# Kernel optimization log

Hardware: AMD Instinct MI355X
Metric: run time of the kernel (lower is better)

Reference implementation:

```python
import jax, jax.numpy as jnp
import numpy as np

N, C, H, W, D = 4, 320, 16, 16, 16
POS_RATIO = 0.5


def setup_inputs() -> dict:
    key = jax.random.key(0)
    k1, k2, k3, k4 = jax.random.split(key, 4)
    q = jax.random.normal(k1, (N, C, H, W, D), jnp.float32)
    k = jax.random.normal(k2, (N, C, H, W, D), jnp.float32)

    def make_coord(kr):
        # crop boxes: upper-left corner in [0, 0.4), extent in [0.4, 0.6)
        start = jax.random.uniform(kr, (N, 3), jnp.float32) * 0.4
        size = 0.4 + jax.random.uniform(jax.random.fold_in(kr, 1), (N, 3), jnp.float32) * 0.2
        return jnp.concatenate([start, start + size], axis=1)  # (N, 6)

    coord_q = make_coord(k3)
    coord_k = make_coord(k4)
    return {"q": q, "k": k, "coord_q": coord_q, "coord_k": coord_k}


def _centers(coord, h, w, d):
    """coord: (N,6) -> centers (N, h*w*d, 3) of each voxel in global coords, and bin diag (N,)."""
    dims = jnp.array([h, w, d], jnp.float32)
    bin_sz = (coord[:, 3:6] - coord[:, 0:3]) / dims  # (N,3) = (bin_h, bin_w, bin_d)
    ax = jnp.arange(h, dtype=jnp.float32) + 0.5
    ay = jnp.arange(w, dtype=jnp.float32) + 0.5
    az = jnp.arange(d, dtype=jnp.float32) + 0.5
    grid = jnp.stack(jnp.meshgrid(ax, ay, az, indexing="ij"), axis=-1)  # (h,w,d,3)
    grid = grid.reshape(1, h * w * d, 3)
    centers = grid * bin_sz[:, None, :] + coord[:, None, 0:3]  # (N, L, 3)
    diag = jnp.sqrt(jnp.sum(bin_sz ** 2, axis=-1))  # (N,)
    return centers, diag


def reference(q, k, coord_q, coord_k):
    n, c, h, w, d = q.shape
    L = h * w * d
    qf = q.reshape(n, c, L)
    kf = k.reshape(n, c, L)

    cq, diag_q = _centers(coord_q, h, w, d)  # (N,L,3), (N,)
    ck, diag_k = _centers(coord_k, h, w, d)
    max_diag = jnp.maximum(diag_q, diag_k)[:, None, None]  # (N,1,1)

    def masked_loss(q_flat, centers_q):
        # pairwise center distance (N, L, L) -- sum of three squared diffs, no (N,L,L,3) stack
        d2 = ((centers_q[:, :, None, 0] - ck[:, None, :, 0]) ** 2
              + (centers_q[:, :, None, 1] - ck[:, None, :, 1]) ** 2
              + (centers_q[:, :, None, 2] - ck[:, None, :, 2]) ** 2)
        dist = jnp.sqrt(d2) / max_diag
        mask = jax.lax.stop_gradient((dist < POS_RATIO).astype(jnp.float32))
        logit = jnp.einsum("ncl,ncm->nlm", q_flat, kf)  # bmm(q^T, k)
        return jnp.sum(logit * mask, axis=(-2, -1)) / (jnp.sum(mask, axis=(-2, -1)) + 1e-6)

    loss = masked_loss(qf, cq)
    # anatomy branch: flip(q) and flipped q-centers along batch dim 0 (as in source flip(x, dim=0))
    loss_rev = masked_loss(jnp.flip(qf, axis=0), jnp.flip(cq, axis=0))
    return -2.0 * jnp.mean(loss) - 2.0 * jnp.mean(loss_rev)
```

## Files before the change

kernel.cpp:

```cpp
#include <hip/hip_runtime.h>

#define LVOX   4096
#define NCH    320
#define NCOMBO 8
#define RCAP   49152
#define PKSTR  17
#define PKROW  (256 * PKSTR)
#define NBLK   (2 * NCH)
#define SPART_OFF 128
#define RUNS_OFF  (SPART_OFF + NCOMBO * NBLK * 4)

struct Geo {
    float qs0, qs1, qs2, qo0, qo1, qo2;
    float ks0, ks1, ks2, ko0, ko1, ko2;
    float ik0, ik1, ik2;
    float T;
};

__device__ __forceinline__ Geo make_geo(const float* __restrict__ cq,
                                        const float* __restrict__ ck,
                                        int n, int qb) {
    Geo g;
    const float* qc = cq + qb * 6;
    const float* qn = cq + n * 6;
    const float* kc = ck + n * 6;
    g.qs0 = (qc[3] - qc[0]) * (1.f / 16.f); g.qo0 = qc[0];
    g.qs1 = (qc[4] - qc[1]) * (1.f / 16.f); g.qo1 = qc[1];
    g.qs2 = (qc[5] - qc[2]) * (1.f / 16.f); g.qo2 = qc[2];
    g.ks0 = (kc[3] - kc[0]) * (1.f / 16.f); g.ko0 = kc[0];
    g.ks1 = (kc[4] - kc[1]) * (1.f / 16.f); g.ko1 = kc[1];
    g.ks2 = (kc[5] - kc[2]) * (1.f / 16.f); g.ko2 = kc[2];
    g.ik0 = 1.f / g.ks0; g.ik1 = 1.f / g.ks1; g.ik2 = 1.f / g.ks2;
    float b0 = (qn[3] - qn[0]) * (1.f / 16.f);
    float b1 = (qn[4] - qn[1]) * (1.f / 16.f);
    float b2 = (qn[5] - qn[2]) * (1.f / 16.f);
    float dq = sqrtf(b0 * b0 + b1 * b1 + b2 * b2);
    float dk = sqrtf(g.ks0 * g.ks0 + g.ks1 * g.ks1 + g.ks2 * g.ks2);
    g.T = 0.5f * fmaxf(dq, dk);
    return g;
}

__device__ __forceinline__ void axrange(float c, float ko, float ik, float T,
                                        int& m0, int& m1) {
    float lo = (c - T - ko) * ik - 0.5f;
    float hi = (c + T - ko) * ik - 0.5f;
    m0 = max((int)ceilf(lo) - 1, 0);
    m1 = min((int)floorf(hi) + 1, 15);
}

__global__ void enum_runs(const float* __restrict__ coord_q,
                          const float* __restrict__ coord_k,
                          unsigned* __restrict__ pcnt,
                          unsigned* __restrict__ rcnt,
                          unsigned* __restrict__ runs, int cap) {
    int gid = blockIdx.x * 256 + threadIdx.x;
    int j = gid >> 12;
    int l = gid & 4095;
    int n = j & 3;
    int qb = (j & 4) ? (3 - n) : n;
    Geo g = make_geo(coord_q, coord_k, n, qb);

    int ix = l >> 8, iy = (l >> 4) & 15, iz = l & 15;
    float cx = (ix + 0.5f) * g.qs0 + g.qo0;
    float cy = (iy + 0.5f) * g.qs1 + g.qo1;
    float cz = (iz + 0.5f) * g.qs2 + g.qo2;
    int x0, x1, y0, y1, z0, z1;
    axrange(cx, g.ko0, g.ik0, g.T, x0, x1);
    axrange(cy, g.ko1, g.ik1, g.T, y0, y1);
    axrange(cz, g.ko2, g.ik2, g.T, z0, z1);

    int nh = 0, nr = 0;
    for (int x = x0; x <= x1; ++x) {
        float dx = cx - ((x + 0.5f) * g.ks0 + g.ko0);
        float dx2 = dx * dx;
        for (int y = y0; y <= y1; ++y) {
            float dy = cy - ((y + 0.5f) * g.ks1 + g.ko1);
            float dxy = dx2 + dy * dy;
            int zc = 0;
            for (int z = z0; z <= z1; ++z) {
                float dz = cz - ((z + 0.5f) * g.ks2 + g.ko2);
                if (sqrtf(dxy + dz * dz) < g.T) zc++;
            }
            if (zc) { nr++; nh += zc; }
        }
    }

    int lane = threadIdx.x & 63;
    int incl = nr;
#pragma unroll
    for (int off = 1; off < 64; off <<= 1) {
        int t = __shfl_up(incl, off, 64);
        if (lane >= off) incl += t;
    }
    int total = __shfl(incl, 63, 64);
    int base = 0;
    if (lane == 63) base = (int)atomicAdd(&rcnt[j], (unsigned)total);
    base = __shfl(base, 63, 64);
    int w = base + incl - nr;

    int hsum = nh;
#pragma unroll
    for (int off = 32; off; off >>= 1) hsum += __shfl_down(hsum, off, 64);
    if (lane == 0) atomicAdd(&pcnt[j], (unsigned)hsum);

    unsigned* out = runs + (size_t)j * (size_t)cap;
    for (int x = x0; x <= x1; ++x) {
        float dx = cx - ((x + 0.5f) * g.ks0 + g.ko0);
        float dx2 = dx * dx;
        for (int y = y0; y <= y1; ++y) {
            float dy = cy - ((y + 0.5f) * g.ks1 + g.ko1);
            float dxy = dx2 + dy * dy;
            int zf = -1, zc = 0;
            for (int z = z0; z <= z1; ++z) {
                float dz = cz - ((z + 0.5f) * g.ks2 + g.ko2);
                if (sqrtf(dxy + dz * dz) < g.T) { if (!zc) zf = z; zc++; }
            }
            if (zc) {
                if (w < cap)
                    out[w] = ((unsigned)l << 16)
                           | ((unsigned)((x << 8) | (y << 4) | zf) << 4)
                           | (unsigned)(zc - 1);
                w++;
            }
        }
    }
}

__global__ void __launch_bounds__(512) gather_fused(
        const float* __restrict__ q, const float* __restrict__ k,
        const unsigned* __restrict__ rcnt, const unsigned* __restrict__ runs,
        int cap, float* __restrict__ Spart) {
    __shared__ float sh[2 * LVOX + 2 * PKROW + 32];
    const int QA = 0, QB = LVOX, PK = 2 * LVOX, SR = 2 * LVOX + 2 * PKROW;

    int g = blockIdx.x;
    int c = blockIdx.y;
    int n0 = g ? 1 : 0;
    int n1 = 3 - n0;
    int t = threadIdx.x;

    const float* q0 = q + ((size_t)(n0 * NCH + c)) * LVOX;
    const float* q1 = q + ((size_t)(n1 * NCH + c)) * LVOX;
#pragma unroll
    for (int i = 0; i < 2; ++i) {
        int off = (t + 512 * i) * 4;
        *(float4*)&sh[QA + off] = *(const float4*)&q0[off];
        *(float4*)&sh[QB + off] = *(const float4*)&q1[off];
    }

    {
        int row = t >> 8;
        int cl  = t & 255;
        const float* ks = k + ((size_t)((row ? n1 : n0) * NCH + c)) * LVOX + cl * 16;
        float4 v0 = *(const float4*)&ks[0];
        float4 v1 = *(const float4*)&ks[4];
        float4 v2 = *(const float4*)&ks[8];
        float4 v3 = *(const float4*)&ks[12];
        float vv[16] = {v0.x, v0.y, v0.z, v0.w, v1.x, v1.y, v1.z, v1.w,
                        v2.x, v2.y, v2.z, v2.w, v3.x, v3.y, v3.z, v3.w};
        float* dst = &sh[PK + row * PKROW + cl * PKSTR];
        float e = 0.f;
        dst[0] = 0.f;
#pragma unroll
        for (int i = 0; i < 16; ++i) { e += vv[i]; dst[i + 1] = e; }
    }
    __syncthreads();

    const int jl[4]   = {n0, n1, 4 + n0, 4 + n1};
    const int qoff[4] = {QA, QB, QB, QA};
    const int koff[4] = {PK, PK + PKROW, PK, PK + PKROW};
    float accv[4];

#pragma unroll
    for (int ci = 0; ci < 4; ++ci) {
        int j = jl[ci];
        unsigned cnt = rcnt[j];
        if (cnt > (unsigned)cap) cnt = (unsigned)cap;
        const unsigned* rl = runs + (size_t)j * (size_t)cap;
        int qb = qoff[ci], kb = koff[ci];
        float acc = 0.f;
        for (unsigned p = (unsigned)t * 4u; p < cnt; p += 512u * 4u) {
            uint4 r4 = *(const uint4*)&rl[p];
            unsigned rr[4] = {r4.x, r4.y, r4.z, r4.w};
#pragma unroll
            for (int e = 0; e < 4; ++e) {
                bool valid = (p + (unsigned)e) < cnt;
                unsigned pr = rr[e];
                int l    = (int)(pr >> 16);
                int cell = (int)((pr >> 8) & 255u);
                int zf   = (int)((pr >> 4) & 15u);
                int len  = (int)(pr & 15u) + 1;
                float s = sh[kb + cell * PKSTR + zf + len] - sh[kb + cell * PKSTR + zf];
                acc += valid ? sh[qb + l] * s : 0.f;
            }
        }
        accv[ci] = acc;
    }

    int wv = t >> 6, lane = t & 63;
#pragma unroll
    for (int ci = 0; ci < 4; ++ci) {
        float a = accv[ci];
#pragma unroll
        for (int off = 32; off; off >>= 1) a += __shfl_down(a, off, 64);
        if (lane == 0) sh[SR + wv * 4 + ci] = a;
    }
    __syncthreads();
    if (t < 4) {
        float v = 0.f;
#pragma unroll
        for (int w = 0; w < 8; ++w) v += sh[SR + w * 4 + t];
        Spart[(size_t)jl[t] * NBLK + (c * 2 + g)] = v;
    }
}

__global__ void finalize(const float* __restrict__ Spart,
                         const unsigned* __restrict__ pcnt,
                         float* __restrict__ out) {
    __shared__ float tj[NCOMBO];
    int j = threadIdx.x >> 5;
    int s = threadIdx.x & 31;
    int nn = j & 3;
    int gj = (nn == 1 || nn == 2) ? 1 : 0;
    float v = 0.f;
    for (int i = s; i < NCH; i += 32)
        v += Spart[(size_t)j * NBLK + i * 2 + gj];
#pragma unroll
    for (int off = 16; off; off >>= 1) v += __shfl_down(v, off, 32);
    if (s == 0) tj[j] = v;
    __syncthreads();
    if (threadIdx.x == 0) {
        float t = 0.f;
#pragma unroll
        for (int jj = 0; jj < NCOMBO; ++jj)
            t += tj[jj] / ((float)pcnt[jj] + 1e-6f);
        out[0] = -0.5f * t;
    }
}

extern "C" void kernel_launch(void* const* d_in, const int* in_sizes, int n_in,
                              void* d_out, int out_size, void* d_ws, size_t ws_size,
                              hipStream_t stream) {
    const float* q       = (const float*)d_in[0];
    const float* k       = (const float*)d_in[1];
    const float* coord_q = (const float*)d_in[2];
    const float* coord_k = (const float*)d_in[3];
    float* out = (float*)d_out;

    unsigned* pcnt  = (unsigned*)d_ws;
    unsigned* rcnt  = (unsigned*)d_ws + 8;
    float*    Spart = (float*)((char*)d_ws + SPART_OFF);
    unsigned* runs  = (unsigned*)((char*)d_ws + RUNS_OFF);

    size_t avail = (ws_size > RUNS_OFF) ? ((ws_size - RUNS_OFF) / 4) / NCOMBO : 4;
    avail &= ~(size_t)3;
    int cap = (int)((avail < (size_t)RCAP) ? avail : (size_t)RCAP);
    if (cap < 4) cap = 4;

    hipMemsetAsync(d_ws, 0, 128, stream);
    enum_runs<<<(NCOMBO * LVOX) / 256, 256, 0, stream>>>(coord_q, coord_k, pcnt, rcnt, runs, cap);
    gather_fused<<<dim3(2, NCH), 512, 0, stream>>>(q, k, rcnt, runs, cap, Spart);
    finalize<<<1, 256, 0, stream>>>(Spart, pcnt, out);
}
```

Baseline: 125.0 us.

## Replace global atomic run compaction with per-wavefront fixed segments

After: 124.6 us. Within noise of the previous version (-0.4%).

```diff
diff --git a/kernel.cpp b/kernel.cpp
--- a/kernel.cpp
+++ b/kernel.cpp
@@ -3,12 +3,14 @@
 #define LVOX   4096
 #define NCH    320
 #define NCOMBO 8
-#define RCAP   49152
+#define NSEG   64
+#define SEGCAP 4096
 #define PKSTR  17
 #define PKROW  (256 * PKSTR)
 #define NBLK   (2 * NCH)
-#define SPART_OFF 128
-#define RUNS_OFF  (SPART_OFF + NCOMBO * NBLK * 4)
+#define WPCNT_OFF 2048
+#define SPART_OFF 4096
+#define RUNS_OFF  24576
 
 struct Geo {
     float qs0, qs1, qs2, qo0, qo1, qo2;
@@ -50,12 +52,13 @@
 
 __global__ void enum_runs(const float* __restrict__ coord_q,
                           const float* __restrict__ coord_k,
-                          unsigned* __restrict__ pcnt,
-                          unsigned* __restrict__ rcnt,
-                          unsigned* __restrict__ runs, int cap) {
+                          unsigned* __restrict__ wcnt,
+                          unsigned* __restrict__ wpcnt,
+                          unsigned* __restrict__ runs) {
     int gid = blockIdx.x * 256 + threadIdx.x;
     int j = gid >> 12;
     int l = gid & 4095;
+    int seg = j * NSEG + ((gid & 4095) >> 6);
     int n = j & 3;
     int qb = (j & 4) ? (3 - n) : n;
     Geo g = make_geo(coord_q, coord_k, n, qb);
@@ -92,18 +95,15 @@
         int t = __shfl_up(incl, off, 64);
         if (lane >= off) incl += t;
     }
-    int total = __shfl(incl, 63, 64);
-    int base = 0;
-    if (lane == 63) base = (int)atomicAdd(&rcnt[j], (unsigned)total);
-    base = __shfl(base, 63, 64);
-    int w = base + incl - nr;
+    int w = incl - nr;
+    if (lane == 63) wcnt[seg] = (unsigned)incl;
 
     int hsum = nh;
 #pragma unroll
     for (int off = 32; off; off >>= 1) hsum += __shfl_down(hsum, off, 64);
-    if (lane == 0) atomicAdd(&pcnt[j], (unsigned)hsum);
-
-    unsigned* out = runs + (size_t)j * (size_t)cap;
+    if (lane == 0) wpcnt[seg] = (unsigned)hsum;
+
+    unsigned* out = runs + (size_t)seg * SEGCAP;
     for (int x = x0; x <= x1; ++x) {
         float dx = cx - ((x + 0.5f) * g.ks0 + g.ko0);
         float dx2 = dx * dx;
@@ -116,7 +116,7 @@
                 if (sqrtf(dxy + dz * dz) < g.T) { if (!zc) zf = z; zc++; }
             }
             if (zc) {
-                if (w < cap)
+                if (w < SEGCAP)
                     out[w] = ((unsigned)l << 16)
                            | ((unsigned)((x << 8) | (y << 4) | zf) << 4)
                            | (unsigned)(zc - 1);
@@ -128,8 +128,8 @@
 
 __global__ void __launch_bounds__(512) gather_fused(
         const float* __restrict__ q, const float* __restrict__ k,
-        const unsigned* __restrict__ rcnt, const unsigned* __restrict__ runs,
-        int cap, float* __restrict__ Spart) {
+        const unsigned* __restrict__ wcnt, const unsigned* __restrict__ runs,
+        float* __restrict__ Spart) {
     __shared__ float sh[2 * LVOX + 2 * PKROW + 32];
     const int QA = 0, QB = LVOX, PK = 2 * LVOX, SR = 2 * LVOX + 2 * PKROW;
 
@@ -171,22 +171,25 @@
     const int koff[4] = {PK, PK + PKROW, PK, PK + PKROW};
     float accv[4];
 
+    int segi = t >> 3;
+    int tin  = t & 7;
+
 #pragma unroll
     for (int ci = 0; ci < 4; ++ci) {
         int j = jl[ci];
-        unsigned cnt = rcnt[j];
-        if (cnt > (unsigned)cap) cnt = (unsigned)cap;
-        const unsigned* rl = runs + (size_t)j * (size_t)cap;
+        unsigned cnt = wcnt[j * NSEG + segi];
+        if (cnt > SEGCAP) cnt = SEGCAP;
+        const unsigned* rl = runs + (size_t)(j * NSEG + segi) * SEGCAP;
         int qb = qoff[ci], kb = koff[ci];
         float acc = 0.f;
-        for (unsigned p = (unsigned)t * 4u; p < cnt; p += 512u * 4u) {
+        for (unsigned p = (unsigned)tin * 4u; p < cnt; p += 32u) {
             uint4 r4 = *(const uint4*)&rl[p];
             unsigned rr[4] = {r4.x, r4.y, r4.z, r4.w};
 #pragma unroll
             for (int e = 0; e < 4; ++e) {
                 bool valid = (p + (unsigned)e) < cnt;
                 unsigned pr = rr[e];
-                int l    = (int)(pr >> 16);
+                int l    = (int)((pr >> 16) & 4095u);
                 int cell = (int)((pr >> 8) & 255u);
                 int zf   = (int)((pr >> 4) & 15u);
                 int len  = (int)(pr & 15u) + 1;
@@ -215,7 +218,7 @@
 }
 
 __global__ void finalize(const float* __restrict__ Spart,
-                         const unsigned* __restrict__ pcnt,
+                         const unsigned* __restrict__ wpcnt,
                          float* __restrict__ out) {
     __shared__ float tj[NCOMBO];
     int j = threadIdx.x >> 5;
@@ -225,15 +228,19 @@
     float v = 0.f;
     for (int i = s; i < NCH; i += 32)
         v += Spart[(size_t)j * NBLK + i * 2 + gj];
-#pragma unroll
-    for (int off = 16; off; off >>= 1) v += __shfl_down(v, off, 32);
-    if (s == 0) tj[j] = v;
+    unsigned pc = wpcnt[j * NSEG + s] + wpcnt[j * NSEG + s + 32];
+    float pcf = (float)pc;
+#pragma unroll
+    for (int off = 16; off; off >>= 1) {
+        v   += __shfl_down(v, off, 32);
+        pcf += __shfl_down(pcf, off, 32);
+    }
+    if (s == 0) tj[j] = v / (pcf + 1e-6f);
     __syncthreads();
     if (threadIdx.x == 0) {
         float t = 0.f;
 #pragma unroll
-        for (int jj = 0; jj < NCOMBO; ++jj)
-            t += tj[jj] / ((float)pcnt[jj] + 1e-6f);
+        for (int jj = 0; jj < NCOMBO; ++jj) t += tj[jj];
         out[0] = -0.5f * t;
     }
 }
@@ -247,18 +254,12 @@
     const float* coord_k = (const float*)d_in[3];
     float* out = (float*)d_out;
 
-    unsigned* pcnt  = (unsigned*)d_ws;
-    unsigned* rcnt  = (unsigned*)d_ws + 8;
+    unsigned* wcnt  = (unsigned*)d_ws;
+    unsigned* wpcnt = (unsigned*)((char*)d_ws + WPCNT_OFF);
     float*    Spart = (float*)((char*)d_ws + SPART_OFF);
     unsigned* runs  = (unsigned*)((char*)d_ws + RUNS_OFF);
 
-    size_t avail = (ws_size > RUNS_OFF) ? ((ws_size - RUNS_OFF) / 4) / NCOMBO : 4;
-    avail &= ~(size_t)3;
-    int cap = (int)((avail < (size_t)RCAP) ? avail : (size_t)RCAP);
-    if (cap < 4) cap = 4;
-
-    hipMemsetAsync(d_ws, 0, 128, stream);
-    enum_runs<<<(NCOMBO * LVOX) / 256, 256, 0, stream>>>(coord_q, coord_k, pcnt, rcnt, runs, cap);
-    gather_fused<<<dim3(2, NCH), 512, 0, stream>>>(q, k, rcnt, runs, cap, Spart);
-    finalize<<<1, 256, 0, stream>>>(Spart, pcnt, out);
-}
+    enum_runs<<<(NCOMBO * LVOX) / 256, 256, 0, stream>>>(coord_q, coord_k, wcnt, wpcnt, runs);
+    gather_fused<<<dim3(2, NCH), 512, 0, stream>>>(q, k, wcnt, runs, Spart);
+    finalize<<<1, 256, 0, stream>>>(Spart, wpcnt, out);
+}
```
